# Optimization experiments

Hardware: AMD Instinct MI355X
Metric: run time of the kernel (lower is better)

Reference implementation:

```python
import jax, jax.numpy as jnp
import numpy as np

H = 5          # hidden units per LSTMCell (hardcoded in source)
F = 64         # input feature dim
T = 100        # seq_len (hardcoded in source)
B = 16384      # batch
OUT = 3        # dense output units


def setup_inputs() -> dict:
    key = jax.random.key(0)
    ks = jax.random.split(key, 12)
    s = 0.1
    return {
        "x":  jax.random.normal(ks[0], (B, T, F), dtype=jnp.float32),
        # layer 1: input F -> hidden H, keras kernel layout [in, 4H] gate order i,f,c,o
        "W1": jax.random.normal(ks[1], (F, 4 * H), dtype=jnp.float32) * s,
        "U1": jax.random.normal(ks[2], (H, 4 * H), dtype=jnp.float32) * s,
        "b1": jax.random.normal(ks[3], (4 * H,), dtype=jnp.float32) * s,
        # layer 2: H -> H
        "W2": jax.random.normal(ks[4], (H, 4 * H), dtype=jnp.float32) * s,
        "U2": jax.random.normal(ks[5], (H, 4 * H), dtype=jnp.float32) * s,
        "b2": jax.random.normal(ks[6], (4 * H,), dtype=jnp.float32) * s,
        # layer 3: H -> H
        "W3": jax.random.normal(ks[7], (H, 4 * H), dtype=jnp.float32) * s,
        "U3": jax.random.normal(ks[8], (H, 4 * H), dtype=jnp.float32) * s,
        "b3": jax.random.normal(ks[9], (4 * H,), dtype=jnp.float32) * s,
        # final dense: H -> OUT
        "Wd": jax.random.normal(ks[10], (H, OUT), dtype=jnp.float32) * s,
        "bd": jax.random.normal(ks[11], (OUT,), dtype=jnp.float32) * s,
    }


def _lstm_layer(seq, W, U, b):
    """Run one keras-style LSTMCell over time. seq: [B,T,Din] -> [B,T,H]."""
    # precompute input contribution for all timesteps: [B,T,4H]
    xz = jnp.einsum("btd,dk->btk", seq, W) + b
    xz_t = jnp.swapaxes(xz, 0, 1)  # [T,B,4H]
    b_sz = seq.shape[0]
    h0 = jnp.zeros((b_sz, H), dtype=seq.dtype)
    c0 = jnp.zeros((b_sz, H), dtype=seq.dtype)

    def step(carry, zx):
        h, c = carry
        z = zx + h @ U  # [B,4H]
        i = jax.nn.sigmoid(z[:, 0 * H:1 * H])
        f = jax.nn.sigmoid(z[:, 1 * H:2 * H])
        g = jnp.tanh(z[:, 2 * H:3 * H])
        o = jax.nn.sigmoid(z[:, 3 * H:4 * H])
        c_new = f * c + i * g
        h_new = o * jnp.tanh(c_new)
        return (h_new, c_new), h_new

    (_, _), hs = jax.lax.scan(step, (h0, c0), xz_t)
    return jnp.swapaxes(hs, 0, 1)  # [B,T,H]


def reference(x, W1, U1, b1, W2, U2, b2, W3, U3, b3, Wd, bd):
    s1 = _lstm_layer(x, W1, U1, b1)    # [B,T,H]
    s2 = _lstm_layer(s1, W2, U2, b2)   # [B,T,H]
    s3 = _lstm_layer(s2, W3, U3, b3)   # [B,T,H]
    last = s3[:, -1, :]                # only final hidden of layer 3 is used
    return last @ Wd + bd              # [B,OUT]
```

## Files before the change

kernel.cpp:

```cpp
#include <hip/hip_runtime.h>
#include <cstddef>

#define BB   16384
#define TT_  100
#define FF   64
#define K4   20
#define NOUT 3

__device__ __forceinline__ float sigf(float x) {
    return __builtin_amdgcn_rcpf(1.0f + __expf(-x));
}
__device__ __forceinline__ float tanhf_fast(float x) {
    return 1.0f - 2.0f * __builtin_amdgcn_rcpf(__expf(2.0f * x) + 1.0f);
}
template <int IMM>
__device__ __forceinline__ float swz(float v) {
    return __int_as_float(__builtin_amdgcn_ds_swizzle(__float_as_int(v), IMM));
}

template <int NT>
__device__ __forceinline__ void rec_steps(
    float (&zbuf)[8][K4][9], int g, int ue,
    const float (&u1w)[4][5], const float (&w2w)[4][5], const float (&u2w)[4][5],
    const float (&w3w)[4][5], const float (&u3w)[4][5],
    const float (&bb1)[4], const float (&bb2)[4], const float (&bb3)[4],
    float (&h1)[5], float (&h2)[5], float (&h3)[5],
    float &c1, float &c2, float &c3)
{
#pragma unroll
    for (int s = 0; s < NT; ++s) {
        float z[4];
#pragma unroll
        for (int j = 0; j < 4; ++j) {
            float acc = zbuf[s][j * 5 + ue][g] + bb1[j];
#pragma unroll
            for (int d = 0; d < 5; ++d) acc = fmaf(h1[d], u1w[j][d], acc);
            z[j] = acc;
        }
        {
            const float iv = sigf(z[0]), fv = sigf(z[1]);
            const float gv = tanhf_fast(z[2]), ov = sigf(z[3]);
            c1 = fmaf(fv, c1, iv * gv);
            const float ho = ov * tanhf_fast(c1);
            h1[0] = swz<0x018>(ho); h1[1] = swz<0x038>(ho);
            h1[2] = swz<0x058>(ho); h1[3] = swz<0x078>(ho);
            h1[4] = swz<0x098>(ho);
        }
#pragma unroll
        for (int j = 0; j < 4; ++j) {
            float acc = bb2[j];
#pragma unroll
            for (int d = 0; d < 5; ++d) acc = fmaf(h1[d], w2w[j][d], acc);
#pragma unroll
            for (int d = 0; d < 5; ++d) acc = fmaf(h2[d], u2w[j][d], acc);
            z[j] = acc;
        }
        {
            const float iv = sigf(z[0]), fv = sigf(z[1]);
            const float gv = tanhf_fast(z[2]), ov = sigf(z[3]);
            c2 = fmaf(fv, c2, iv * gv);
            const float ho = ov * tanhf_fast(c2);
            h2[0] = swz<0x018>(ho); h2[1] = swz<0x038>(ho);
            h2[2] = swz<0x058>(ho); h2[3] = swz<0x078>(ho);
            h2[4] = swz<0x098>(ho);
        }
#pragma unroll
        for (int j = 0; j < 4; ++j) {
            float acc = bb3[j];
#pragma unroll
            for (int d = 0; d < 5; ++d) acc = fmaf(h2[d], w3w[j][d], acc);
#pragma unroll
            for (int d = 0; d < 5; ++d) acc = fmaf(h3[d], u3w[j][d], acc);
            z[j] = acc;
        }
        {
            const float iv = sigf(z[0]), fv = sigf(z[1]);
            const float gv = tanhf_fast(z[2]), ov = sigf(z[3]);
            c3 = fmaf(fv, c3, iv * gv);
            const float ho = ov * tanhf_fast(c3);
            h3[0] = swz<0x018>(ho); h3[1] = swz<0x038>(ho);
            h3[2] = swz<0x058>(ho); h3[3] = swz<0x078>(ho);
            h3[4] = swz<0x098>(ho);
        }
    }
}

__global__ __launch_bounds__(64) __attribute__((amdgpu_waves_per_eu(2, 2)))
void fused_lstm_kernel(
    const float* __restrict__ x,
    const float* __restrict__ W1, const float* __restrict__ U1, const float* __restrict__ b1,
    const float* __restrict__ W2, const float* __restrict__ U2, const float* __restrict__ b2,
    const float* __restrict__ W3, const float* __restrict__ U3, const float* __restrict__ b3,
    const float* __restrict__ Wd, const float* __restrict__ bd,
    float* __restrict__ out)
{
    __shared__ float sWT[K4][FF];
    __shared__ float zbuf[8][K4][9];

    const int lane = threadIdx.x;
    const int g    = lane >> 3;
    const int u    = lane & 7;
    const int ue   = (u < 5) ? u : 4;
    const int tq   = (lane >> 1) & 3;
    const int fh   = lane & 1;
    const int b    = blockIdx.x * 8 + g;

    const float* xp0 = x + ((size_t)b * TT_ + tq) * FF + fh * 32;
    const float* xp1 = xp0 + 4 * FF;
    float4 xa0[8], xa1[8];
#pragma unroll
    for (int fc = 0; fc < 8; ++fc) xa0[fc] = ((const float4*)xp0)[fc];
#pragma unroll
    for (int fc = 0; fc < 8; ++fc) xa1[fc] = ((const float4*)xp1)[fc];

#pragma unroll
    for (int w = 0; w < 20; ++w) {
        int i = w * 64 + lane;
        sWT[i % K4][i / K4] = W1[i];
    }

    float u1w[4][5], w2w[4][5], u2w[4][5], w3w[4][5], u3w[4][5];
    float bb1[4], bb2[4], bb3[4];
#pragma unroll
    for (int j = 0; j < 4; ++j) {
        const int k = j * 5 + ue;
#pragma unroll
        for (int d = 0; d < 5; ++d) {
            u1w[j][d] = U1[d * K4 + k];
            w2w[j][d] = W2[d * K4 + k];
            u2w[j][d] = U2[d * K4 + k];
            w3w[j][d] = W3[d * K4 + k];
            u3w[j][d] = U3[d * K4 + k];
        }
        bb1[j] = b1[k];
        bb2[j] = b2[k];
        bb3[j] = b3[k];
    }
    const int uo = (u < NOUT) ? u : 0;
    float wdw[5];
    const float bdw = bd[uo];
#pragma unroll
    for (int d = 0; d < 5; ++d) wdw[d] = Wd[d * NOUT + uo];

    float h1[5] = {0,0,0,0,0}, h2[5] = {0,0,0,0,0}, h3[5] = {0,0,0,0,0};
    float c1 = 0.f, c2 = 0.f, c3 = 0.f;

    const int t1 = tq + (fh << 2);

    for (int c = 0; c < 13; ++c) {
#pragma unroll 4
        for (int k = 0; k < K4; ++k) {
            float a0 = 0.f, a1 = 0.f;
#pragma unroll
            for (int fc = 0; fc < 8; ++fc) {
                const float4 wv = *(const float4*)&sWT[k][fh * 32 + fc * 4];
                const float4 x0 = xa0[fc];
                const float4 x1 = xa1[fc];
                a0 = fmaf(x0.x, wv.x, fmaf(x0.y, wv.y, fmaf(x0.z, wv.z, fmaf(x0.w, wv.w, a0))));
                a1 = fmaf(x1.x, wv.x, fmaf(x1.y, wv.y, fmaf(x1.z, wv.z, fmaf(x1.w, wv.w, a1))));
            }
            a0 += swz<0x041F>(a0);
            a1 += swz<0x041F>(a1);
            zbuf[t1][k][g] = fh ? a1 : a0;
        }

        if (c < 12) {
            xp0 += 8 * FF;
            xp1 = (c == 11) ? xp0 : (xp1 + 8 * FF);
#pragma unroll
            for (int fc = 0; fc < 8; ++fc) xa0[fc] = ((const float4*)xp0)[fc];
#pragma unroll
            for (int fc = 0; fc < 8; ++fc) xa1[fc] = ((const float4*)xp1)[fc];
        }

        if (c < 12) {
            rec_steps<8>(zbuf, g, ue, u1w, w2w, u2w, w3w, u3w,
                         bb1, bb2, bb3, h1, h2, h3, c1, c2, c3);
        } else {
            rec_steps<4>(zbuf, g, ue, u1w, w2w, u2w, w3w, u3w,
                         bb1, bb2, bb3, h1, h2, h3, c1, c2, c3);
        }
    }

    if (u < NOUT) {
        float s = bdw;
#pragma unroll
        for (int d = 0; d < 5; ++d) s = fmaf(h3[d], wdw[d], s);
        out[b * NOUT + u] = s;
    }
}

extern "C" void kernel_launch(void* const* d_in, const int* in_sizes, int n_in,
                              void* d_out, int out_size, void* d_ws, size_t ws_size,
                              hipStream_t stream) {
    const float* x   = (const float*)d_in[0];
    const float* W1  = (const float*)d_in[1];
    const float* U1  = (const float*)d_in[2];
    const float* b1  = (const float*)d_in[3];
    const float* W2  = (const float*)d_in[4];
    const float* U2  = (const float*)d_in[5];
    const float* b2  = (const float*)d_in[6];
    const float* W3  = (const float*)d_in[7];
    const float* U3  = (const float*)d_in[8];
    const float* b3  = (const float*)d_in[9];
    const float* Wd  = (const float*)d_in[10];
    const float* bdp = (const float*)d_in[11];
    float* out = (float*)d_out;

    fused_lstm_kernel<<<BB / 8, 64, 0, stream>>>(
        x, W1, U1, b1, W2, U2, b2, W3, U3, b3, Wd, bdp, out);
}
```

Before: 626.9 us.

## Skew the three LSTM layers in time so their recurrences overlap

```diff
diff --git a/kernel.cpp b/kernel.cpp
--- a/kernel.cpp
+++ b/kernel.cpp
@@ -7,6 +7,9 @@
 #define K4   20
 #define NOUT 3
 
+typedef float ZBUF[8][K4][9];
+typedef float HIST[8][64];
+
 __device__ __forceinline__ float sigf(float x) {
     return __builtin_amdgcn_rcpf(1.0f + __expf(-x));
 }
@@ -17,18 +20,35 @@
 __device__ __forceinline__ float swz(float v) {
     return __int_as_float(__builtin_amdgcn_ds_swizzle(__float_as_int(v), IMM));
 }
-
-template <int NT>
-__device__ __forceinline__ void rec_steps(
-    float (&zbuf)[8][K4][9], int g, int ue,
+__device__ __forceinline__ void lstm_act(const float (&z)[4], float& c, float& ho) {
+    const float iv = sigf(z[0]), fv = sigf(z[1]);
+    const float gv = tanhf_fast(z[2]), ov = sigf(z[3]);
+    c = fmaf(fv, c, iv * gv);
+    ho = ov * tanhf_fast(c);
+}
+
+template <bool D1, bool D2, bool D3>
+__device__ __forceinline__ void pipe_step(
+    int s, ZBUF& zbuf, HIST& h1hist, HIST& h2hist,
+    int g, int ue, int lane,
     const float (&u1w)[4][5], const float (&w2w)[4][5], const float (&u2w)[4][5],
     const float (&w3w)[4][5], const float (&u3w)[4][5],
     const float (&bb1)[4], const float (&bb2)[4], const float (&bb3)[4],
     float (&h1)[5], float (&h2)[5], float (&h3)[5],
-    float &c1, float &c2, float &c3)
-{
-#pragma unroll
-    for (int s = 0; s < NT; ++s) {
+    float& c1, float& c2, float& c3)
+{
+    float nh1[5], nh2[5];
+    if (D2) {
+#pragma unroll
+        for (int d = 0; d < 5; ++d) nh1[d] = h1hist[s][g * 8 + d];
+    }
+    if (D3) {
+#pragma unroll
+        for (int d = 0; d < 5; ++d) nh2[d] = h2hist[s][g * 8 + d];
+    }
+
+    float ho1, ho2, ho3;
+    if (D1) {
         float z[4];
 #pragma unroll
         for (int j = 0; j < 4; ++j) {
@@ -37,52 +57,83 @@
             for (int d = 0; d < 5; ++d) acc = fmaf(h1[d], u1w[j][d], acc);
             z[j] = acc;
         }
-        {
-            const float iv = sigf(z[0]), fv = sigf(z[1]);
-            const float gv = tanhf_fast(z[2]), ov = sigf(z[3]);
-            c1 = fmaf(fv, c1, iv * gv);
-            const float ho = ov * tanhf_fast(c1);
-            h1[0] = swz<0x018>(ho); h1[1] = swz<0x038>(ho);
-            h1[2] = swz<0x058>(ho); h1[3] = swz<0x078>(ho);
-            h1[4] = swz<0x098>(ho);
-        }
+        lstm_act(z, c1, ho1);
+    }
+    if (D2) {
+        float z[4];
 #pragma unroll
         for (int j = 0; j < 4; ++j) {
             float acc = bb2[j];
 #pragma unroll
-            for (int d = 0; d < 5; ++d) acc = fmaf(h1[d], w2w[j][d], acc);
+            for (int d = 0; d < 5; ++d) acc = fmaf(nh1[d], w2w[j][d], acc);
 #pragma unroll
             for (int d = 0; d < 5; ++d) acc = fmaf(h2[d], u2w[j][d], acc);
             z[j] = acc;
         }
-        {
-            const float iv = sigf(z[0]), fv = sigf(z[1]);
-            const float gv = tanhf_fast(z[2]), ov = sigf(z[3]);
-            c2 = fmaf(fv, c2, iv * gv);
-            const float ho = ov * tanhf_fast(c2);
-            h2[0] = swz<0x018>(ho); h2[1] = swz<0x038>(ho);
-            h2[2] = swz<0x058>(ho); h2[3] = swz<0x078>(ho);
-            h2[4] = swz<0x098>(ho);
-        }
+        lstm_act(z, c2, ho2);
+    }
+    if (D3) {
+        float z[4];
 #pragma unroll
         for (int j = 0; j < 4; ++j) {
             float acc = bb3[j];
 #pragma unroll
-            for (int d = 0; d < 5; ++d) acc = fmaf(h2[d], w3w[j][d], acc);
+            for (int d = 0; d < 5; ++d) acc = fmaf(nh2[d], w3w[j][d], acc);
 #pragma unroll
             for (int d = 0; d < 5; ++d) acc = fmaf(h3[d], u3w[j][d], acc);
             z[j] = acc;
         }
-        {
-            const float iv = sigf(z[0]), fv = sigf(z[1]);
-            const float gv = tanhf_fast(z[2]), ov = sigf(z[3]);
-            c3 = fmaf(fv, c3, iv * gv);
-            const float ho = ov * tanhf_fast(c3);
-            h3[0] = swz<0x018>(ho); h3[1] = swz<0x038>(ho);
-            h3[2] = swz<0x058>(ho); h3[3] = swz<0x078>(ho);
-            h3[4] = swz<0x098>(ho);
-        }
-    }
+        lstm_act(z, c3, ho3);
+    }
+
+    if (D1) {
+        h1hist[s][lane] = ho1;
+        h1[0] = swz<0x018>(ho1); h1[1] = swz<0x038>(ho1);
+        h1[2] = swz<0x058>(ho1); h1[3] = swz<0x078>(ho1);
+        h1[4] = swz<0x098>(ho1);
+    }
+    if (D2) {
+        h2hist[s][lane] = ho2;
+        h2[0] = swz<0x018>(ho2); h2[1] = swz<0x038>(ho2);
+        h2[2] = swz<0x058>(ho2); h2[3] = swz<0x078>(ho2);
+        h2[4] = swz<0x098>(ho2);
+    }
+    if (D3) {
+        h3[0] = swz<0x018>(ho3); h3[1] = swz<0x038>(ho3);
+        h3[2] = swz<0x058>(ho3); h3[3] = swz<0x078>(ho3);
+        h3[4] = swz<0x098>(ho3);
+    }
+}
+
+__device__ __forceinline__ void proj_chunk(
+    const float (&sWT)[K4][FF], ZBUF& zbuf,
+    const float4 (&xa0)[8], const float4 (&xa1)[8],
+    int fh, int t1, int g)
+{
+#pragma unroll 4
+    for (int k = 0; k < K4; ++k) {
+        float a0 = 0.f, a1 = 0.f;
+#pragma unroll
+        for (int fc = 0; fc < 8; ++fc) {
+            const float4 wv = *(const float4*)&sWT[k][fh * 32 + fc * 4];
+            const float4 x0 = xa0[fc];
+            const float4 x1 = xa1[fc];
+            a0 = fmaf(x0.x, wv.x, fmaf(x0.y, wv.y, fmaf(x0.z, wv.z, fmaf(x0.w, wv.w, a0))));
+            a1 = fmaf(x1.x, wv.x, fmaf(x1.y, wv.y, fmaf(x1.z, wv.z, fmaf(x1.w, wv.w, a1))));
+        }
+        a0 += swz<0x041F>(a0);
+        a1 += swz<0x041F>(a1);
+        zbuf[t1][k][g] = fh ? a1 : a0;
+    }
+}
+
+__device__ __forceinline__ void load_x(const float* p0, const float* p1,
+                                       float4 (&xa0)[8], float4 (&xa1)[8])
+{
+#pragma unroll
+    for (int fc = 0; fc < 8; ++fc) xa0[fc] = ((const float4*)p0)[fc];
+#pragma unroll
+    for (int fc = 0; fc < 8; ++fc) xa1[fc] = ((const float4*)p1)[fc];
 }
 
 __global__ __launch_bounds__(64) __attribute__((amdgpu_waves_per_eu(2, 2)))
@@ -95,7 +146,9 @@
     float* __restrict__ out)
 {
     __shared__ float sWT[K4][FF];
-    __shared__ float zbuf[8][K4][9];
+    __shared__ ZBUF zbuf;
+    __shared__ HIST h1hist;
+    __shared__ HIST h2hist;
 
     const int lane = threadIdx.x;
     const int g    = lane >> 3;
@@ -104,14 +157,12 @@
     const int tq   = (lane >> 1) & 3;
     const int fh   = lane & 1;
     const int b    = blockIdx.x * 8 + g;
+    const int t1   = tq + (fh << 2);
 
     const float* xp0 = x + ((size_t)b * TT_ + tq) * FF + fh * 32;
     const float* xp1 = xp0 + 4 * FF;
     float4 xa0[8], xa1[8];
-#pragma unroll
-    for (int fc = 0; fc < 8; ++fc) xa0[fc] = ((const float4*)xp0)[fc];
-#pragma unroll
-    for (int fc = 0; fc < 8; ++fc) xa1[fc] = ((const float4*)xp1)[fc];
+    load_x(xp0, xp1, xa0, xa1);
 
 #pragma unroll
     for (int w = 0; w < 20; ++w) {
@@ -145,48 +196,58 @@
     float h1[5] = {0,0,0,0,0}, h2[5] = {0,0,0,0,0}, h3[5] = {0,0,0,0,0};
     float c1 = 0.f, c2 = 0.f, c3 = 0.f;
 
-    const int t1 = tq + (fh << 2);
-
-    for (int c = 0; c < 13; ++c) {
-#pragma unroll 4
-        for (int k = 0; k < K4; ++k) {
-            float a0 = 0.f, a1 = 0.f;
-#pragma unroll
-            for (int fc = 0; fc < 8; ++fc) {
-                const float4 wv = *(const float4*)&sWT[k][fh * 32 + fc * 4];
-                const float4 x0 = xa0[fc];
-                const float4 x1 = xa1[fc];
-                a0 = fmaf(x0.x, wv.x, fmaf(x0.y, wv.y, fmaf(x0.z, wv.z, fmaf(x0.w, wv.w, a0))));
-                a1 = fmaf(x1.x, wv.x, fmaf(x1.y, wv.y, fmaf(x1.z, wv.z, fmaf(x1.w, wv.w, a1))));
-            }
-            a0 += swz<0x041F>(a0);
-            a1 += swz<0x041F>(a1);
-            zbuf[t1][k][g] = fh ? a1 : a0;
-        }
-
-        if (c < 12) {
-            xp0 += 8 * FF;
-            xp1 = (c == 11) ? xp0 : (xp1 + 8 * FF);
-#pragma unroll
-            for (int fc = 0; fc < 8; ++fc) xa0[fc] = ((const float4*)xp0)[fc];
-#pragma unroll
-            for (int fc = 0; fc < 8; ++fc) xa1[fc] = ((const float4*)xp1)[fc];
-        }
-
-        if (c < 12) {
-            rec_steps<8>(zbuf, g, ue, u1w, w2w, u2w, w3w, u3w,
-                         bb1, bb2, bb3, h1, h2, h3, c1, c2, c3);
-        } else {
-            rec_steps<4>(zbuf, g, ue, u1w, w2w, u2w, w3w, u3w,
-                         bb1, bb2, bb3, h1, h2, h3, c1, c2, c3);
-        }
-    }
+#define STEP(D1, D2, D3, S)                                                   \
+    pipe_step<D1, D2, D3>(S, zbuf, h1hist, h2hist, g, ue, lane,               \
+                          u1w, w2w, u2w, w3w, u3w, bb1, bb2, bb3,             \
+                          h1, h2, h3, c1, c2, c3)
+
+#define PREFETCH(p)                                                           \
+    do {                                                                      \
+        xp0 += 8 * FF;                                                        \
+        xp1 = ((p) == 11) ? xp0 : (xp1 + 8 * FF);             \
+        load_x(xp0, xp1, xa0, xa1);                                           \
+    } while (0)
+
+    proj_chunk(sWT, zbuf, xa0, xa1, fh, t1, g);
+    PREFETCH(0);
+#pragma unroll
+    for (int s = 0; s < 8; ++s) STEP(true, false, false, s);
+
+    proj_chunk(sWT, zbuf, xa0, xa1, fh, t1, g);
+    PREFETCH(1);
+#pragma unroll
+    for (int s = 0; s < 8; ++s) STEP(true, true, false, s);
+
+#pragma unroll 1
+    for (int p = 2; p < 12; ++p) {
+        proj_chunk(sWT, zbuf, xa0, xa1, fh, t1, g);
+        PREFETCH(p);
+#pragma unroll
+        for (int s = 0; s < 8; ++s) STEP(true, true, true, s);
+    }
+
+    proj_chunk(sWT, zbuf, xa0, xa1, fh, t1, g);
+#pragma unroll
+    for (int s = 0; s < 4; ++s) STEP(true, true, true, s);
+#pragma unroll
+    for (int s = 4; s < 8; ++s) STEP(false, true, true, s);
+
+#pragma unroll
+    for (int s = 0; s < 4; ++s) STEP(false, true, true, s);
+#pragma unroll
+    for (int s = 4; s < 8; ++s) STEP(false, false, true, s);
+
+#pragma unroll
+    for (int s = 0; s < 4; ++s) STEP(false, false, true, s);
+
+#undef STEP
+#undef PREFETCH
 
     if (u < NOUT) {
-        float s = bdw;
-#pragma unroll
-        for (int d = 0; d < 5; ++d) s = fmaf(h3[d], wdw[d], s);
-        out[b * NOUT + u] = s;
+        float sacc = bdw;
+#pragma unroll
+        for (int d = 0; d < 5; ++d) sacc = fmaf(h3[d], wdw[d], sacc);
+        out[b * NOUT + u] = sacc;
     }
 }
 
```

New measurement: 638.7 us. Within noise of the previous version (+1.9%).

## Give each lane a whole timestep and read transposed W1 from global memory

Applied to the files above, without the earlier changes.

```diff
diff --git a/kernel.cpp b/kernel.cpp
--- a/kernel.cpp
+++ b/kernel.cpp
@@ -7,6 +7,8 @@
 #define K4   20
 #define NOUT 3
 
+typedef float ZBUF[8][8][28];
+
 __device__ __forceinline__ float sigf(float x) {
     return __builtin_amdgcn_rcpf(1.0f + __expf(-x));
 }
@@ -20,7 +22,7 @@
 
 template <int NT>
 __device__ __forceinline__ void rec_steps(
-    float (&zbuf)[8][K4][9], int g, int ue,
+    ZBUF& zbuf, int g, int ue,
     const float (&u1w)[4][5], const float (&w2w)[4][5], const float (&u2w)[4][5],
     const float (&w3w)[4][5], const float (&u3w)[4][5],
     const float (&bb1)[4], const float (&bb2)[4], const float (&bb3)[4],
@@ -32,7 +34,7 @@
         float z[4];
 #pragma unroll
         for (int j = 0; j < 4; ++j) {
-            float acc = zbuf[s][j * 5 + ue][g] + bb1[j];
+            float acc = zbuf[s][g][j * 5 + ue] + bb1[j];
 #pragma unroll
             for (int d = 0; d < 5; ++d) acc = fmaf(h1[d], u1w[j][d], acc);
             z[j] = acc;
@@ -85,38 +87,39 @@
     }
 }
 
+__global__ void prep_w1t(const float* __restrict__ W1, float* __restrict__ W1T) {
+    int i = blockIdx.x * 256 + threadIdx.x;
+    if (i < 13 * 1280) {
+        int j = i % 1280;
+        int k = j / 64, f = j % 64;
+        W1T[i] = W1[f * K4 + k];
+    }
+}
+
 __global__ __launch_bounds__(64) __attribute__((amdgpu_waves_per_eu(2, 2)))
 void fused_lstm_kernel(
     const float* __restrict__ x,
-    const float* __restrict__ W1, const float* __restrict__ U1, const float* __restrict__ b1,
+    const float* __restrict__ W1T,
+    const float* __restrict__ U1, const float* __restrict__ b1,
     const float* __restrict__ W2, const float* __restrict__ U2, const float* __restrict__ b2,
     const float* __restrict__ W3, const float* __restrict__ U3, const float* __restrict__ b3,
     const float* __restrict__ Wd, const float* __restrict__ bd,
     float* __restrict__ out)
 {
-    __shared__ float sWT[K4][FF];
-    __shared__ float zbuf[8][K4][9];
+    __shared__ ZBUF zbuf;
 
     const int lane = threadIdx.x;
     const int g    = lane >> 3;
     const int u    = lane & 7;
     const int ue   = (u < 5) ? u : 4;
-    const int tq   = (lane >> 1) & 3;
-    const int fh   = lane & 1;
+    const int tq   = lane & 7;
     const int b    = blockIdx.x * 8 + g;
 
-    const float* xp0 = x + ((size_t)b * TT_ + tq) * FF + fh * 32;
-    const float* xp1 = xp0 + 4 * FF;
-    float4 xa0[8], xa1[8];
-#pragma unroll
-    for (int fc = 0; fc < 8; ++fc) xa0[fc] = ((const float4*)xp0)[fc];
-#pragma unroll
-    for (int fc = 0; fc < 8; ++fc) xa1[fc] = ((const float4*)xp1)[fc];
-
-#pragma unroll
-    for (int w = 0; w < 20; ++w) {
-        int i = w * 64 + lane;
-        sWT[i % K4][i / K4] = W1[i];
+    float4 xa[16];
+    {
+        const float* xp = x + ((size_t)b * TT_ + tq) * FF;
+#pragma unroll
+        for (int fc = 0; fc < 16; ++fc) xa[fc] = ((const float4*)xp)[fc];
     }
 
     float u1w[4][5], w2w[4][5], u2w[4][5], w3w[4][5], u3w[4][5];
@@ -145,32 +148,38 @@
     float h1[5] = {0,0,0,0,0}, h2[5] = {0,0,0,0,0}, h3[5] = {0,0,0,0,0};
     float c1 = 0.f, c2 = 0.f, c3 = 0.f;
 
-    const int t1 = tq + (fh << 2);
-
+#pragma unroll 1
     for (int c = 0; c < 13; ++c) {
-#pragma unroll 4
-        for (int k = 0; k < K4; ++k) {
-            float a0 = 0.f, a1 = 0.f;
-#pragma unroll
-            for (int fc = 0; fc < 8; ++fc) {
-                const float4 wv = *(const float4*)&sWT[k][fh * 32 + fc * 4];
-                const float4 x0 = xa0[fc];
-                const float4 x1 = xa1[fc];
-                a0 = fmaf(x0.x, wv.x, fmaf(x0.y, wv.y, fmaf(x0.z, wv.z, fmaf(x0.w, wv.w, a0))));
-                a1 = fmaf(x1.x, wv.x, fmaf(x1.y, wv.y, fmaf(x1.z, wv.z, fmaf(x1.w, wv.w, a1))));
+        const float* Wc = W1T + c * 1280;
+#pragma unroll
+        for (int kq = 0; kq < 5; ++kq) {
+            float acc[4];
+#pragma unroll
+            for (int i = 0; i < 4; ++i) acc[i] = b1[kq * 4 + i];
+#pragma unroll
+            for (int i = 0; i < 4; ++i) acc[i] = 0.f;
+#pragma unroll
+            for (int fc = 0; fc < 16; ++fc) {
+                const float4 xv = xa[fc];
+#pragma unroll
+                for (int i = 0; i < 4; ++i) {
+                    const float4 wv = *(const float4*)(Wc + (kq * 4 + i) * FF + fc * 4);
+                    acc[i] = fmaf(xv.x, wv.x,
+                             fmaf(xv.y, wv.y,
+                             fmaf(xv.z, wv.z,
+                             fmaf(xv.w, wv.w, acc[i]))));
+                }
             }
-            a0 += swz<0x041F>(a0);
-            a1 += swz<0x041F>(a1);
-            zbuf[t1][k][g] = fh ? a1 : a0;
+            *(float4*)&zbuf[tq][g][kq * 4] =
+                make_float4(acc[0], acc[1], acc[2], acc[3]);
         }
 
         if (c < 12) {
-            xp0 += 8 * FF;
-            xp1 = (c == 11) ? xp0 : (xp1 + 8 * FF);
-#pragma unroll
-            for (int fc = 0; fc < 8; ++fc) xa0[fc] = ((const float4*)xp0)[fc];
-#pragma unroll
-            for (int fc = 0; fc < 8; ++fc) xa1[fc] = ((const float4*)xp1)[fc];
+            int tn = (c + 1) * 8 + tq;
+            if (tn > TT_ - 1) tn = TT_ - 1;
+            const float* xp = x + ((size_t)b * TT_ + tn) * FF;
+#pragma unroll
+            for (int fc = 0; fc < 16; ++fc) xa[fc] = ((const float4*)xp)[fc];
         }
 
         if (c < 12) {
@@ -183,10 +192,10 @@
     }
 
     if (u < NOUT) {
-        float s = bdw;
-#pragma unroll
-        for (int d = 0; d < 5; ++d) s = fmaf(h3[d], wdw[d], s);
-        out[b * NOUT + u] = s;
+        float sacc = bdw;
+#pragma unroll
+        for (int d = 0; d < 5; ++d) sacc = fmaf(h3[d], wdw[d], sacc);
+        out[b * NOUT + u] = sacc;
     }
 }
 
@@ -206,7 +215,9 @@
     const float* Wd  = (const float*)d_in[10];
     const float* bdp = (const float*)d_in[11];
     float* out = (float*)d_out;
-
+    float* W1T = (float*)d_ws;
+
+    prep_w1t<<<(13 * 1280 + 255) / 256, 256, 0, stream>>>(W1, W1T);
     fused_lstm_kernel<<<BB / 8, 64, 0, stream>>>(
-        x, W1, U1, b1, W2, U2, b2, W3, U3, b3, Wd, bdp, out);
-}
+        x, W1T, U1, b1, W2, U2, b2, W3, U3, b3, Wd, bdp, out);
+}
```

Result: slower. 753.2 us (+20.1%).
